# Kernel optimization log

Hardware: AMD Instinct MI355X
Metric: run time of the kernel (lower is better)

Reference implementation:

```python
import jax, jax.numpy as jnp
import numpy as np
from jax import lax

THRESH = 0.8
LENS = 0.4
DECAY = 0.2
LOG_SIG_MIN, LOG_SIG_MAX = -20.0, 2.0
WINS = 15

@jax.custom_vjp
def act_fun(x):
    return (x > THRESH).astype(x.dtype)

def _act_fwd(x):
    return act_fun(x), x

def _act_bwd(x, g):
    return (g * (jnp.abs(x - THRESH) < LENS).astype(g.dtype),)

act_fun.defvjp(_act_fwd, _act_bwd)

B, NIN, HID, NACT = 2048, 512, 1024, 32

def _xavier(key, out_d, in_d):
    lim = jnp.sqrt(6.0 / (in_d + out_d)).astype(jnp.float32)
    return jax.random.uniform(key, (out_d, in_d), jnp.float32, -lim, lim)

def setup_inputs() -> dict:
    key = jax.random.key(0)
    ks = jax.random.split(key, 12)
    inp = {
        'state': jax.random.normal(ks[0], (B, 5, NIN), jnp.float32),
        'w1': _xavier(ks[1], HID, NIN), 'b1': jnp.zeros((HID,), jnp.float32),
        'w2': _xavier(ks[2], HID, NIN), 'b2': jnp.zeros((HID,), jnp.float32),
        'w3': _xavier(ks[3], HID, NIN), 'b3': jnp.zeros((HID,), jnp.float32),
        'wl': _xavier(ks[4], 1, 3), 'bl': jnp.zeros((1,), jnp.float32),
        'w11': _xavier(ks[5], HID, 4 * HID), 'b11': jnp.zeros((HID,), jnp.float32),
        'w12': _xavier(ks[6], HID, HID), 'b12': jnp.zeros((HID,), jnp.float32),
        'w21': _xavier(ks[7], HID, 4 * HID), 'b21': jnp.zeros((HID,), jnp.float32),
        'w22': _xavier(ks[8], HID, HID), 'b22': jnp.zeros((HID,), jnp.float32),
        'wm': _xavier(ks[9], NACT, HID), 'bm': jnp.zeros((NACT,), jnp.float32),
        'ws': _xavier(ks[10], NACT, HID), 'bs': jnp.zeros((NACT,), jnp.float32),
    }
    return inp

def _policy_forward(state, w1, b1, w2, b2, w3, b3, wl, bl,
                    w11, b11, w12, b12, w21, b21, w22, b22, wm, bm, ws, bs):
    batch = state.shape[0]
    hid = w1.shape[0]
    seq = jnp.repeat(state, 3, axis=1)
    mem0 = jnp.zeros((batch, hid, 4), state.dtype)
    sp0 = jnp.zeros((batch, hid, 4), state.dtype)

    def step(carry, x_t):
        mem, spike = carry
        i1 = x_t @ w1.T + b1  # [B, HID]
        i2 = x_t @ w2.T + b2
        i3 = x_t @ w3.T + b3
        inner = jnp.einsum('bck,k->bc', mem[:, :, :3], wl[0]) + bl[0]
        inp_all = jnp.stack([i1, i2, i3, inner], axis=-1)  # [B, HID, 4]
        mem1 = mem * DECAY * (1.0 - spike) + inp_all
        sp1 = act_fun(mem1)
        return (mem1, sp1), sp1

    _, spikes = lax.scan(step, (mem0, sp0), jnp.swapaxes(seq, 0, 1))  # [T,B,HID,4]
    spikes = jnp.transpose(spikes, (1, 0, 2, 3)).reshape(batch, WINS, hid * 4)
    x = jnp.mean(spikes, axis=1)  # [B, 4*HID]

    x1 = jax.nn.relu(x @ w11.T + b11)
    x1 = jax.nn.relu(x1 @ w12.T + b12)
    mean = x1 @ wm.T + bm

    x2 = jax.nn.relu(x @ w21.T + b21)
    x2 = jax.nn.relu(x2 @ w22.T + b22)
    log_std = jnp.clip(x2 @ ws.T + bs, LOG_SIG_MIN, LOG_SIG_MAX)
    return mean, log_std

def reference(state, w1, b1, w2, b2, w3, b3, wl, bl,
              w11, b11, w12, b12, w21, b21, w22, b22, wm, bm, ws, bs):
    return _policy_forward(state, w1, b1, w2, b2, w3, b3, wl, bl,
                           w11, b11, w12, b12, w21, b21, w22, b22, wm, bm, ws, bs)
```

## Files before the change

### kernel.cpp

```cpp
#include <hip/hip_runtime.h>
#include <cstddef>
#include <cstdint>

#define THRESH 0.8f
#define DECAY  0.2f

typedef unsigned short ushort_t;
typedef __attribute__((ext_vector_type(8))) short bf16x8;
typedef __attribute__((ext_vector_type(4))) float f32x4;
typedef __attribute__((ext_vector_type(4))) int i32x4;

__device__ __forceinline__ ushort_t f2bf(float f) {
    union { float f; unsigned u; } v; v.f = f;
    unsigned r = v.u + 0x7FFFu + ((v.u >> 16) & 1u);
    return (ushort_t)(r >> 16);
}
__device__ __forceinline__ float bf2f(ushort_t h) {
    union { unsigned u; float f; } v; v.u = ((unsigned)h) << 16;
    return v.f;
}
__device__ __forceinline__ float blo(unsigned u) {
    union { unsigned x; float f; } v; v.x = u << 16; return v.f;
}
__device__ __forceinline__ float bhi(unsigned u) {
    union { unsigned x; float f; } v; v.x = u & 0xFFFF0000u; return v.f;
}

__device__ __forceinline__ void gload16(const void* g, void* l) {
    __builtin_amdgcn_global_load_lds(
        (const __attribute__((address_space(1))) void*)g,
        (__attribute__((address_space(3))) void*)l,
        16, 0, 0);
}


__global__ __launch_bounds__(512) void cur_gemm512(
    const ushort_t* __restrict__ Ah, const ushort_t* __restrict__ Al,
    const ushort_t* __restrict__ Wh, const ushort_t* __restrict__ Wl,
    const float* __restrict__ bias, float* __restrict__ C,
    int K, int ldc)
{
    __shared__ ushort_t sA[2][128 * 32];
    __shared__ ushort_t sW[2][128 * 32];

    const int t = threadIdx.x;
    const int mBase = blockIdx.x * 128;
    const int nBase = blockIdx.y * 128;

    const int lane = t & 63;
    const int wv = t >> 6;
    const int wm = (wv & 1) * 64;
    const int wn = (wv >> 1) * 32;
    const int fr = lane & 15;
    const int fq = lane >> 4;
    const int fsw = (fq ^ ((fr >> 1) & 3)) * 8;

    const int r0 = t >> 2;
    const int cc = ((t & 3) ^ ((t >> 3) & 3)) * 8;

    f32x4 acc[4][2];
#pragma unroll
    for (int i = 0; i < 4; i++)
#pragma unroll
        for (int j = 0; j < 2; j++) {
            f32x4 z = {0.f, 0.f, 0.f, 0.f};
            acc[i][j] = z;
        }

    for (int k0 = 0; k0 < K; k0 += 32) {
        const int lin = t * 8;
        gload16(&Ah[(size_t)(mBase + r0) * K + k0 + cc], &sA[0][lin]);
        gload16(&Wh[(size_t)(nBase + r0) * K + k0 + cc], &sW[0][lin]);
        gload16(&Al[(size_t)(mBase + r0) * K + k0 + cc], &sA[1][lin]);
        gload16(&Wl[(size_t)(nBase + r0) * K + k0 + cc], &sW[1][lin]);
        __syncthreads();

        bf16x8 af[4][2], wf[2][2];
#pragma unroll
        for (int s = 0; s < 2; s++) {
#pragma unroll
            for (int i = 0; i < 4; i++)
                af[i][s] = *(const bf16x8*)&sA[s][(wm + i * 16 + fr) * 32 + fsw];
#pragma unroll
            for (int j = 0; j < 2; j++)
                wf[j][s] = *(const bf16x8*)&sW[s][(wn + j * 16 + fr) * 32 + fsw];
        }
#pragma unroll
        for (int i = 0; i < 4; i++)
#pragma unroll
            for (int j = 0; j < 2; j++) {
                acc[i][j] = __builtin_amdgcn_mfma_f32_16x16x32_bf16(af[i][0], wf[j][0], acc[i][j], 0, 0, 0);
                acc[i][j] = __builtin_amdgcn_mfma_f32_16x16x32_bf16(af[i][0], wf[j][1], acc[i][j], 0, 0, 0);
                acc[i][j] = __builtin_amdgcn_mfma_f32_16x16x32_bf16(af[i][1], wf[j][0], acc[i][j], 0, 0, 0);
            }
        __syncthreads();
    }

#pragma unroll
    for (int j = 0; j < 2; j++) {
        const int col = nBase + wn + j * 16 + fr;
        const float bv = bias[col];
#pragma unroll
        for (int i = 0; i < 4; i++)
#pragma unroll
            for (int r = 0; r < 4; r++) {
                const int row = mBase + wm + i * 16 + fq * 4 + r;
                C[(size_t)row * ldc + col] = acc[i][j][r] + bv;
            }
    }
}

__global__ __launch_bounds__(256) void mlp1_i8(
    const signed char* __restrict__ A, const signed char* __restrict__ W,
    const float* __restrict__ wsc, const float* __restrict__ bias,
    ushort_t* __restrict__ C)
{
    __shared__ signed char sA[64 * 64];
    __shared__ signed char sW[128 * 64];

    const int t = threadIdx.x;
    const int mBase = blockIdx.x * 64;
    const int nBase = blockIdx.y * 128;

    const int lane = t & 63;
    const int wv = t >> 6;
    const int wn = wv * 32;
    const int fr = lane & 15;
    const int fq = lane >> 4;
    const int fsw = (fq ^ ((fr >> 1) & 3)) * 16;

    const int r0 = t >> 2;
    const int cc = ((t & 3) ^ ((t >> 3) & 3)) * 16;

    i32x4 acc[4][2];
#pragma unroll
    for (int i = 0; i < 4; i++)
#pragma unroll
        for (int j = 0; j < 2; j++) {
            i32x4 z = {0, 0, 0, 0};
            acc[i][j] = z;
        }

    for (int k0 = 0; k0 < 4096; k0 += 64) {
        gload16(&A[(size_t)(mBase + r0) * 4096 + k0 + cc], &sA[t * 16]);
        gload16(&W[(size_t)(nBase + r0) * 4096 + k0 + cc], &sW[t * 16]);
        gload16(&W[(size_t)(nBase + 64 + r0) * 4096 + k0 + cc], &sW[4096 + t * 16]);
        __syncthreads();

        i32x4 af[4], wf[2];
#pragma unroll
        for (int i = 0; i < 4; i++)
            af[i] = *(const i32x4*)&sA[(i * 16 + fr) * 64 + fsw];
#pragma unroll
        for (int j = 0; j < 2; j++)
            wf[j] = *(const i32x4*)&sW[(wn + j * 16 + fr) * 64 + fsw];
#pragma unroll
        for (int i = 0; i < 4; i++)
#pragma unroll
            for (int j = 0; j < 2; j++)
                acc[i][j] = __builtin_amdgcn_mfma_i32_16x16x64_i8(af[i], wf[j], acc[i][j], 0, 0, 0);
        __syncthreads();
    }

#pragma unroll
    for (int j = 0; j < 2; j++) {
        const int col = nBase + wn + j * 16 + fr;
        const float sc = wsc[col];
        const float bv = bias[col];
#pragma unroll
        for (int i = 0; i < 4; i++)
#pragma unroll
            for (int r = 0; r < 4; r++) {
                const int row = mBase + i * 16 + fq * 4 + r;
                const float v = (float)acc[i][j][r] * sc + bv;
                C[(size_t)row * 2048 + col] = f2bf(fmaxf(v, 0.f));
            }
    }
}

__global__ __launch_bounds__(256) void mlp2_bf16(
    const ushort_t* __restrict__ A, const ushort_t* __restrict__ W,
    const float* __restrict__ bias, ushort_t* __restrict__ C,
    int N, int K, int lda, int ldw, int ldc, int aHalfOff)
{
    __shared__ ushort_t sA[64 * 32];
    __shared__ ushort_t sW[128 * 32];

    const int t = threadIdx.x;
    const int mBase = blockIdx.x * 64;
    const int nBase = blockIdx.y * 128;
    const int aOff = (2 * nBase >= N) ? aHalfOff : 0;

    const int lane = t & 63;
    const int wv = t >> 6;
    const int wn = wv * 32;
    const int fr = lane & 15;
    const int fq = lane >> 4;
    const int fsw = (fq ^ ((fr >> 1) & 3)) * 8;

    const int r0 = t >> 2;
    const int cc = ((t & 3) ^ ((t >> 3) & 3)) * 8;

    f32x4 acc[4][2];
#pragma unroll
    for (int i = 0; i < 4; i++)
#pragma unroll
        for (int j = 0; j < 2; j++) {
            f32x4 z = {0.f, 0.f, 0.f, 0.f};
            acc[i][j] = z;
        }

    for (int k0 = 0; k0 < K; k0 += 32) {
        gload16(&A[(size_t)(mBase + r0) * lda + aOff + k0 + cc], &sA[t * 8]);
        gload16(&W[(size_t)(nBase + r0) * ldw + k0 + cc], &sW[t * 8]);
        gload16(&W[(size_t)(nBase + 64 + r0) * ldw + k0 + cc], &sW[2048 + t * 8]);
        __syncthreads();

        bf16x8 af[4], wf[2];
#pragma unroll
        for (int i = 0; i < 4; i++)
            af[i] = *(const bf16x8*)&sA[(i * 16 + fr) * 32 + fsw];
#pragma unroll
        for (int j = 0; j < 2; j++)
            wf[j] = *(const bf16x8*)&sW[(wn + j * 16 + fr) * 32 + fsw];
#pragma unroll
        for (int i = 0; i < 4; i++)
#pragma unroll
            for (int j = 0; j < 2; j++)
                acc[i][j] = __builtin_amdgcn_mfma_f32_16x16x32_bf16(af[i], wf[j], acc[i][j], 0, 0, 0);
        __syncthreads();
    }

#pragma unroll
    for (int j = 0; j < 2; j++) {
        const int col = nBase + wn + j * 16 + fr;
        const float bv = bias[col];
#pragma unroll
        for (int i = 0; i < 4; i++)
#pragma unroll
            for (int r = 0; r < 4; r++) {
                const int row = mBase + i * 16 + fq * 4 + r;
                C[(size_t)row * ldc + col] = f2bf(fmaxf(acc[i][j][r] + bv, 0.f));
            }
    }
}

__global__ __launch_bounds__(256) void recur_kernel(
    const float* __restrict__ cur, const float* __restrict__ wl,
    const float* __restrict__ bl, signed char* __restrict__ x)
{
    const int idx = blockIdx.x * 256 + threadIdx.x;
    const int b = idx >> 10, c = idx & 1023;
    const float wl0 = wl[0], wl1 = wl[1], wl2 = wl[2], bl0 = bl[0];
    float m0 = 0, m1 = 0, m2 = 0, m3 = 0;
    int s0 = 0, s1 = 0, s2 = 0, s3 = 0;
#pragma unroll
    for (int f = 0; f < 5; f++) {
        const float* p = cur + (size_t)(b * 5 + f) * 3072 + c;
        const float i1 = p[0], i2 = p[1024], i3 = p[2048];
#pragma unroll
        for (int rep = 0; rep < 3; rep++) {
            const float inner = m0 * wl0 + m1 * wl1 + m2 * wl2 + bl0;
            const float n0 = i1 + ((m0 > THRESH) ? 0.f : DECAY * m0);
            const float n1 = i2 + ((m1 > THRESH) ? 0.f : DECAY * m1);
            const float n2 = i3 + ((m2 > THRESH) ? 0.f : DECAY * m2);
            const float n3 = inner + ((m3 > THRESH) ? 0.f : DECAY * m3);
            m0 = n0; m1 = n1; m2 = n2; m3 = n3;
            s0 += (n0 > THRESH); s1 += (n1 > THRESH);
            s2 += (n2 > THRESH); s3 += (n3 > THRESH);
        }
    }
    uchar4 o;
    o.x = (unsigned char)s0; o.y = (unsigned char)s1;
    o.z = (unsigned char)s2; o.w = (unsigned char)s3;
    *(uchar4*)&x[(size_t)b * 4096 + c * 4] = o;
}

__device__ __forceinline__ void do_split4(const float4* src, ushort4* hi,
                                          ushort4* lo, int base, int t) {
#pragma unroll
    for (int p = 0; p < 4; p++) {
        const int i = base * 1024 + p * 256 + t;
        const float4 v = src[i];
        ushort4 h, l;
        h.x = f2bf(v.x); l.x = f2bf(v.x - bf2f(h.x));
        h.y = f2bf(v.y); l.y = f2bf(v.y - bf2f(h.y));
        h.z = f2bf(v.z); l.z = f2bf(v.z - bf2f(h.z));
        h.w = f2bf(v.w); l.w = f2bf(v.w - bf2f(h.w));
        hi[i] = h; lo[i] = l;
    }
}
__device__ __forceinline__ void do_cvt4(const float4* src, ushort4* dst,
                                        int base, int t) {
#pragma unroll
    for (int p = 0; p < 4; p++) {
        const int i = base * 1024 + p * 256 + t;
        const float4 v = src[i];
        ushort4 h;
        h.x = f2bf(v.x); h.y = f2bf(v.y); h.z = f2bf(v.z); h.w = f2bf(v.w);
        dst[i] = h;
    }
}
__device__ __forceinline__ int q8(float x, float inv) {
    int q = (int)rintf(x * inv);
    q = q > 127 ? 127 : (q < -127 ? -127 : q);
    return q & 0xff;
}

__global__ __launch_bounds__(256) void prep_kernel(
    const float* __restrict__ state,
    const float* __restrict__ w1, const float* __restrict__ w2,
    const float* __restrict__ w3,
    const float* __restrict__ w11, const float* __restrict__ w21,
    const float* __restrict__ w12, const float* __restrict__ w22,
    const float* __restrict__ b1, const float* __restrict__ b2,
    const float* __restrict__ b3, const float* __restrict__ b11,
    const float* __restrict__ b21, const float* __restrict__ b12,
    const float* __restrict__ b22,
    ushort_t* __restrict__ sh, ushort_t* __restrict__ sl,
    ushort_t* __restrict__ wh123, ushort_t* __restrict__ wl123,
    signed char* __restrict__ w1q, float* __restrict__ wsc,
    ushort_t* __restrict__ w2b,
    float* __restrict__ b123, float* __restrict__ bb1, float* __restrict__ bb2)
{
    const int bid = blockIdx.x;
    const int t = threadIdx.x;
    if (bid < 1280) {
        do_split4((const float4*)state, (ushort4*)sh, (ushort4*)sl, bid, t);
    } else if (bid < 1408) {
        do_split4((const float4*)w1, (ushort4*)wh123, (ushort4*)wl123, bid - 1280, t);
    } else if (bid < 1536) {
        do_split4((const float4*)w2, (ushort4*)(wh123 + 524288),
                  (ushort4*)(wl123 + 524288), bid - 1408, t);
    } else if (bid < 1664) {
        do_split4((const float4*)w3, (ushort4*)(wh123 + 1048576),
                  (ushort4*)(wl123 + 1048576), bid - 1536, t);
    } else if (bid < 3712) {
        const int r = bid - 1664;
        const float* src = (r < 1024) ? (w11 + (size_t)r * 4096)
                                      : (w21 + (size_t)(r - 1024) * 4096);
        __shared__ float red[256];
        float4 v[4];
        float lmax = 0.f;
#pragma unroll
        for (int p = 0; p < 4; p++) {
            v[p] = ((const float4*)src)[t * 4 + p];
            lmax = fmaxf(lmax, fmaxf(fmaxf(fabsf(v[p].x), fabsf(v[p].y)),
                                     fmaxf(fabsf(v[p].z), fabsf(v[p].w))));
        }
        red[t] = lmax;
        __syncthreads();
        for (int s = 128; s > 0; s >>= 1) {
            if (t < s) red[t] = fmaxf(red[t], red[t + s]);
            __syncthreads();
        }
        const float gmax = fmaxf(red[0], 1e-30f);
        const float inv = 127.0f / gmax;
        int4 o;
        o.x = q8(v[0].x, inv) | (q8(v[0].y, inv) << 8) | (q8(v[0].z, inv) << 16) | (q8(v[0].w, inv) << 24);
        o.y = q8(v[1].x, inv) | (q8(v[1].y, inv) << 8) | (q8(v[1].z, inv) << 16) | (q8(v[1].w, inv) << 24);
        o.z = q8(v[2].x, inv) | (q8(v[2].y, inv) << 8) | (q8(v[2].z, inv) << 16) | (q8(v[2].w, inv) << 24);
        o.w = q8(v[3].x, inv) | (q8(v[3].y, inv) << 8) | (q8(v[3].z, inv) << 16) | (q8(v[3].w, inv) << 24);
        ((int4*)(w1q + (size_t)r * 4096))[t] = o;
        if (t == 0) wsc[r] = gmax / (127.0f * 15.0f);
    } else if (bid < 3968) {
        do_cvt4((const float4*)w12, (ushort4*)w2b, bid - 3712, t);
    } else if (bid < 4224) {
        do_cvt4((const float4*)w22, (ushort4*)(w2b + 1048576), bid - 3968, t);
    } else {
#pragma unroll
        for (int p = 0; p < 4; p++) {
            const int i = p * 256 + t;
            b123[i] = b1[i]; b123[1024 + i] = b2[i]; b123[2048 + i] = b3[i];
            bb1[i] = b11[i]; bb1[1024 + i] = b21[i];
            bb2[i] = b12[i]; bb2[1024 + i] = b22[i];
        }
    }
}

__global__ __launch_bounds__(256) void head_kernel(
    const ushort_t* __restrict__ h, const float* __restrict__ wm,
    const float* __restrict__ bm, const float* __restrict__ ws,
    const float* __restrict__ bs, float* __restrict__ out)
{
    const int t = threadIdx.x;
    const int branch = blockIdx.x >> 8;
    const int n = t & 31;
    const int b = (blockIdx.x & 255) * 8 + (t >> 5);
    const ushort_t* hr = h + (size_t)b * 2048 + branch * 1024;
    const float* wr = (branch ? ws : wm) + (size_t)n * 1024;
    float s = 0.f;
#pragma unroll 4
    for (int k = 0; k < 1024; k += 8) {
        const uint4 hv = *(const uint4*)&hr[k];
        const float4 w0 = *(const float4*)&wr[k];
        const float4 w1 = *(const float4*)&wr[k + 4];
        s += blo(hv.x) * w0.x + bhi(hv.x) * w0.y
           + blo(hv.y) * w0.z + bhi(hv.y) * w0.w
           + blo(hv.z) * w1.x + bhi(hv.z) * w1.y
           + blo(hv.w) * w1.z + bhi(hv.w) * w1.w;
    }
    s += (branch ? bs : bm)[n];
    if (branch) s = fminf(fmaxf(s, -20.f), 2.f);
    out[(size_t)branch * 65536 + (size_t)b * 32 + n] = s;
}

extern "C" void kernel_launch(void* const* d_in, const int* in_sizes, int n_in,
                              void* d_out, int out_size, void* d_ws, size_t ws_size,
                              hipStream_t stream)
{
    const float* state = (const float*)d_in[0];
    const float* w1  = (const float*)d_in[1];  const float* b1  = (const float*)d_in[2];
    const float* w2  = (const float*)d_in[3];  const float* b2  = (const float*)d_in[4];
    const float* w3  = (const float*)d_in[5];  const float* b3  = (const float*)d_in[6];
    const float* wl  = (const float*)d_in[7];  const float* bl  = (const float*)d_in[8];
    const float* w11 = (const float*)d_in[9];  const float* b11 = (const float*)d_in[10];
    const float* w12 = (const float*)d_in[11]; const float* b12 = (const float*)d_in[12];
    const float* w21 = (const float*)d_in[13]; const float* b21 = (const float*)d_in[14];
    const float* w22 = (const float*)d_in[15]; const float* b22 = (const float*)d_in[16];
    const float* wm  = (const float*)d_in[17]; const float* bm  = (const float*)d_in[18];
    const float* ws  = (const float*)d_in[19]; const float* bs  = (const float*)d_in[20];
    float* out = (float*)d_out;

    char* wp = (char*)d_ws;
    float*       cur   = (float*)wp;       wp += (size_t)10240 * 3072 * 4;
    ushort_t*    sh    = (ushort_t*)wp;    wp += (size_t)10240 * 512 * 2;
    ushort_t*    sl    = (ushort_t*)wp;    wp += (size_t)10240 * 512 * 2;
    ushort_t*    wh123 = (ushort_t*)wp;    wp += (size_t)3072 * 512 * 2;
    ushort_t*    wl123 = (ushort_t*)wp;    wp += (size_t)3072 * 512 * 2;
    signed char* xb    = (signed char*)wp; wp += (size_t)2048 * 4096;
    signed char* w1q   = (signed char*)wp; wp += (size_t)2048 * 4096;
    ushort_t*    w2b   = (ushort_t*)wp;    wp += (size_t)2048 * 1024 * 2;
    ushort_t*    h1    = (ushort_t*)wp;    wp += (size_t)2048 * 2048 * 2;
    ushort_t*    h2    = (ushort_t*)wp;    wp += (size_t)2048 * 2048 * 2;
    float*       wsc   = (float*)wp;       wp += 2048 * 4;
    float*       b123  = (float*)wp;       wp += 3072 * 4;
    float*       bb1   = (float*)wp;       wp += 2048 * 4;
    float*       bb2   = (float*)wp;       wp += 2048 * 4;

    prep_kernel<<<4225, 256, 0, stream>>>(
        state, w1, w2, w3, w11, w21, w12, w22,
        b1, b2, b3, b11, b21, b12, b22,
        sh, sl, wh123, wl123, w1q, wsc, w2b, b123, bb1, bb2);

    cur_gemm512<<<dim3(80, 24), 512, 0, stream>>>(
        sh, sl, wh123, wl123, b123, cur, 512, 3072);

    recur_kernel<<<8192, 256, 0, stream>>>(cur, wl, bl, xb);

    mlp1_i8<<<dim3(32, 16), 256, 0, stream>>>(xb, w1q, wsc, bb1, h1);

    mlp2_bf16<<<dim3(32, 16), 256, 0, stream>>>(
        h1, w2b, bb2, h2, 2048, 1024, 2048, 1024, 2048, 1024);

    head_kernel<<<512, 256, 0, stream>>>(h2, wm, bm, ws, bs, out);
}
```

Measured before the change: 380.2 us.

## Fold split-bf16 terms into K dimension and use 256x256 pipelined GEMM tile

The prep kernel now writes the state and weight hi/lo bf16 splits as one concatenated K=1536 row each, arranged as [h,h,l] against [h,l,h]. This lets a single bf16 GEMM compute the three-term error-compensated product. The cur GEMM moves from 128x128 tiles to 256x256 tiles with 8 waves. It uses a 4-slot LDS ring loaded via global_load_lds, two tiles in flight, explicit vmcnt waits, and setprio around the MFMA block. The aim is more data reuse per LDS load and overlap of loads with compute, at the cost of a 3x larger A workspace to write and read, and higher register and LDS use (128KB LDS per block).

```diff
diff --git a/kernel.cpp b/kernel.cpp
--- a/kernel.cpp
+++ b/kernel.cpp
@@ -33,79 +33,92 @@
         16, 0, 0);
 }
 
-
-__global__ __launch_bounds__(512) void cur_gemm512(
-    const ushort_t* __restrict__ Ah, const ushort_t* __restrict__ Al,
-    const ushort_t* __restrict__ Wh, const ushort_t* __restrict__ Wl,
-    const float* __restrict__ bias, float* __restrict__ C,
-    int K, int ldc)
-{
-    __shared__ ushort_t sA[2][128 * 32];
-    __shared__ ushort_t sW[2][128 * 32];
+__global__ __launch_bounds__(512, 2) void cur_gemm_qb(
+    const ushort_t* __restrict__ A, const ushort_t* __restrict__ W,
+    const float* __restrict__ bias, float* __restrict__ C)
+{
+    __shared__ ushort_t lds[4][16384];
 
     const int t = threadIdx.x;
-    const int mBase = blockIdx.x * 128;
-    const int nBase = blockIdx.y * 128;
+    const int mBase = blockIdx.x * 256;
+    const int nBase = blockIdx.y * 256;
 
     const int lane = t & 63;
     const int wv = t >> 6;
-    const int wm = (wv & 1) * 64;
-    const int wn = (wv >> 1) * 32;
+    const int wm = (wv >> 2) * 128;
+    const int wn = (wv & 3) * 64;
     const int fr = lane & 15;
     const int fq = lane >> 4;
     const int fsw = (fq ^ ((fr >> 1) & 3)) * 8;
 
     const int r0 = t >> 2;
-    const int cc = ((t & 3) ^ ((t >> 3) & 3)) * 8;
-
-    f32x4 acc[4][2];
-#pragma unroll
-    for (int i = 0; i < 4; i++)
-#pragma unroll
-        for (int j = 0; j < 2; j++) {
+    const int sc0 = ((t & 3) ^ ((r0 >> 1) & 3)) * 8;
+    const size_t aRow0 = (size_t)(mBase + r0) * 1536 + sc0;
+    const size_t aRow1 = (size_t)(mBase + r0 + 128) * 1536 + sc0;
+    const size_t wRow0 = (size_t)(nBase + r0) * 1536 + sc0;
+    const size_t wRow1 = (size_t)(nBase + r0 + 128) * 1536 + sc0;
+
+    f32x4 acc[8][4];
+#pragma unroll
+    for (int i = 0; i < 8; i++)
+#pragma unroll
+        for (int j = 0; j < 4; j++) {
             f32x4 z = {0.f, 0.f, 0.f, 0.f};
             acc[i][j] = z;
         }
 
-    for (int k0 = 0; k0 < K; k0 += 32) {
-        const int lin = t * 8;
-        gload16(&Ah[(size_t)(mBase + r0) * K + k0 + cc], &sA[0][lin]);
-        gload16(&Wh[(size_t)(nBase + r0) * K + k0 + cc], &sW[0][lin]);
-        gload16(&Al[(size_t)(mBase + r0) * K + k0 + cc], &sA[1][lin]);
-        gload16(&Wl[(size_t)(nBase + r0) * K + k0 + cc], &sW[1][lin]);
-        __syncthreads();
-
-        bf16x8 af[4][2], wf[2][2];
-#pragma unroll
-        for (int s = 0; s < 2; s++) {
-#pragma unroll
-            for (int i = 0; i < 4; i++)
-                af[i][s] = *(const bf16x8*)&sA[s][(wm + i * 16 + fr) * 32 + fsw];
-#pragma unroll
-            for (int j = 0; j < 2; j++)
-                wf[j][s] = *(const bf16x8*)&sW[s][(wn + j * 16 + fr) * 32 + fsw];
-        }
-#pragma unroll
-        for (int i = 0; i < 4; i++)
-#pragma unroll
-            for (int j = 0; j < 2; j++) {
-                acc[i][j] = __builtin_amdgcn_mfma_f32_16x16x32_bf16(af[i][0], wf[j][0], acc[i][j], 0, 0, 0);
-                acc[i][j] = __builtin_amdgcn_mfma_f32_16x16x32_bf16(af[i][0], wf[j][1], acc[i][j], 0, 0, 0);
-                acc[i][j] = __builtin_amdgcn_mfma_f32_16x16x32_bf16(af[i][1], wf[j][0], acc[i][j], 0, 0, 0);
-            }
-        __syncthreads();
-    }
-
-#pragma unroll
-    for (int j = 0; j < 2; j++) {
+#define STAGE(tile)                                                   \
+    do {                                                              \
+        const int k0_ = (tile) * 32;                                  \
+        ushort_t* lb_ = &lds[(tile) & 3][0];                          \
+        gload16(&A[aRow0 + k0_], &lb_[t * 8]);                        \
+        gload16(&A[aRow1 + k0_], &lb_[4096 + t * 8]);                 \
+        gload16(&W[wRow0 + k0_], &lb_[8192 + t * 8]);                 \
+        gload16(&W[wRow1 + k0_], &lb_[12288 + t * 8]);                \
+    } while (0)
+
+    STAGE(0);
+    STAGE(1);
+
+    for (int tt = 0; tt < 48; ++tt) {
+        if (tt < 47) {
+            asm volatile("s_waitcnt vmcnt(4)" ::: "memory");
+        } else {
+            asm volatile("s_waitcnt vmcnt(0)" ::: "memory");
+        }
+        __builtin_amdgcn_s_barrier();
+        __builtin_amdgcn_sched_barrier(0);
+        if (tt < 46) STAGE(tt + 2);
+
+        const ushort_t* lb = &lds[tt & 3][0];
+        bf16x8 af[8], wf[4];
+#pragma unroll
+        for (int i = 0; i < 8; i++)
+            af[i] = *(const bf16x8*)&lb[(wm + i * 16 + fr) * 32 + fsw];
+#pragma unroll
+        for (int j = 0; j < 4; j++)
+            wf[j] = *(const bf16x8*)&lb[8192 + (wn + j * 16 + fr) * 32 + fsw];
+
+        __builtin_amdgcn_s_setprio(1);
+#pragma unroll
+        for (int i = 0; i < 8; i++)
+#pragma unroll
+            for (int j = 0; j < 4; j++)
+                acc[i][j] = __builtin_amdgcn_mfma_f32_16x16x32_bf16(af[i], wf[j], acc[i][j], 0, 0, 0);
+        __builtin_amdgcn_s_setprio(0);
+    }
+#undef STAGE
+
+#pragma unroll
+    for (int j = 0; j < 4; j++) {
         const int col = nBase + wn + j * 16 + fr;
         const float bv = bias[col];
 #pragma unroll
-        for (int i = 0; i < 4; i++)
+        for (int i = 0; i < 8; i++)
 #pragma unroll
             for (int r = 0; r < 4; r++) {
                 const int row = mBase + wm + i * 16 + fq * 4 + r;
-                C[(size_t)row * ldc + col] = acc[i][j][r] + bv;
+                C[(size_t)row * 3072 + col] = acc[i][j][r] + bv;
             }
     }
 }
@@ -276,8 +289,8 @@
     *(uchar4*)&x[(size_t)b * 4096 + c * 4] = o;
 }
 
-__device__ __forceinline__ void do_split4(const float4* src, ushort4* hi,
-                                          ushort4* lo, int base, int t) {
+__device__ __forceinline__ void split_state(const float4* src, ushort4* dst,
+                                            int base, int t) {
 #pragma unroll
     for (int p = 0; p < 4; p++) {
         const int i = base * 1024 + p * 256 + t;
@@ -287,7 +300,25 @@
         h.y = f2bf(v.y); l.y = f2bf(v.y - bf2f(h.y));
         h.z = f2bf(v.z); l.z = f2bf(v.z - bf2f(h.z));
         h.w = f2bf(v.w); l.w = f2bf(v.w - bf2f(h.w));
-        hi[i] = h; lo[i] = l;
+        const int r = i >> 7, c = i & 127;
+        ushort4* row = dst + (size_t)r * 384;
+        row[c] = h; row[128 + c] = h; row[256 + c] = l;
+    }
+}
+__device__ __forceinline__ void split_w(const float4* src, ushort4* dst,
+                                        int base, int t, int roff) {
+#pragma unroll
+    for (int p = 0; p < 4; p++) {
+        const int i = base * 1024 + p * 256 + t;
+        const float4 v = src[i];
+        ushort4 h, l;
+        h.x = f2bf(v.x); l.x = f2bf(v.x - bf2f(h.x));
+        h.y = f2bf(v.y); l.y = f2bf(v.y - bf2f(h.y));
+        h.z = f2bf(v.z); l.z = f2bf(v.z - bf2f(h.z));
+        h.w = f2bf(v.w); l.w = f2bf(v.w - bf2f(h.w));
+        const int r = (i >> 7) + roff, c = i & 127;
+        ushort4* row = dst + (size_t)r * 384;
+        row[c] = h; row[128 + c] = l; row[256 + c] = h;
     }
 }
 __device__ __forceinline__ void do_cvt4(const float4* src, ushort4* dst,
@@ -317,8 +348,7 @@
     const float* __restrict__ b3, const float* __restrict__ b11,
     const float* __restrict__ b21, const float* __restrict__ b12,
     const float* __restrict__ b22,
-    ushort_t* __restrict__ sh, ushort_t* __restrict__ sl,
-    ushort_t* __restrict__ wh123, ushort_t* __restrict__ wl123,
+    ushort_t* __restrict__ Ap, ushort_t* __restrict__ Wp,
     signed char* __restrict__ w1q, float* __restrict__ wsc,
     ushort_t* __restrict__ w2b,
     float* __restrict__ b123, float* __restrict__ bb1, float* __restrict__ bb2)
@@ -326,15 +356,13 @@
     const int bid = blockIdx.x;
     const int t = threadIdx.x;
     if (bid < 1280) {
-        do_split4((const float4*)state, (ushort4*)sh, (ushort4*)sl, bid, t);
+        split_state((const float4*)state, (ushort4*)Ap, bid, t);
     } else if (bid < 1408) {
-        do_split4((const float4*)w1, (ushort4*)wh123, (ushort4*)wl123, bid - 1280, t);
+        split_w((const float4*)w1, (ushort4*)Wp, bid - 1280, t, 0);
     } else if (bid < 1536) {
-        do_split4((const float4*)w2, (ushort4*)(wh123 + 524288),
-                  (ushort4*)(wl123 + 524288), bid - 1408, t);
+        split_w((const float4*)w2, (ushort4*)Wp, bid - 1408, t, 1024);
     } else if (bid < 1664) {
-        do_split4((const float4*)w3, (ushort4*)(wh123 + 1048576),
-                  (ushort4*)(wl123 + 1048576), bid - 1536, t);
+        split_w((const float4*)w3, (ushort4*)Wp, bid - 1536, t, 2048);
     } else if (bid < 3712) {
         const int r = bid - 1664;
         const float* src = (r < 1024) ? (w11 + (size_t)r * 4096)
@@ -424,10 +452,8 @@
 
     char* wp = (char*)d_ws;
     float*       cur   = (float*)wp;       wp += (size_t)10240 * 3072 * 4;
-    ushort_t*    sh    = (ushort_t*)wp;    wp += (size_t)10240 * 512 * 2;
-    ushort_t*    sl    = (ushort_t*)wp;    wp += (size_t)10240 * 512 * 2;
-    ushort_t*    wh123 = (ushort_t*)wp;    wp += (size_t)3072 * 512 * 2;
-    ushort_t*    wl123 = (ushort_t*)wp;    wp += (size_t)3072 * 512 * 2;
+    ushort_t*    Ap    = (ushort_t*)wp;    wp += (size_t)10240 * 1536 * 2;
+    ushort_t*    Wp    = (ushort_t*)wp;    wp += (size_t)3072 * 1536 * 2;
     signed char* xb    = (signed char*)wp; wp += (size_t)2048 * 4096;
     signed char* w1q   = (signed char*)wp; wp += (size_t)2048 * 4096;
     ushort_t*    w2b   = (ushort_t*)wp;    wp += (size_t)2048 * 1024 * 2;
@@ -441,10 +467,9 @@
     prep_kernel<<<4225, 256, 0, stream>>>(
         state, w1, w2, w3, w11, w21, w12, w22,
         b1, b2, b3, b11, b21, b12, b22,
-        sh, sl, wh123, wl123, w1q, wsc, w2b, b123, bb1, bb2);
-
-    cur_gemm512<<<dim3(80, 24), 512, 0, stream>>>(
-        sh, sl, wh123, wl123, b123, cur, 512, 3072);
+        Ap, Wp, w1q, wsc, w2b, b123, bb1, bb2);
+
+    cur_gemm_qb<<<dim3(40, 12), 512, 0, stream>>>(Ap, Wp, b123, cur);
 
     recur_kernel<<<8192, 256, 0, stream>>>(cur, wl, bl, xb);
 
```

Measured after the change: 379.1 us. No clear change (-0.3%).
